# Performance work log

Measured on AMD Instinct MI355X. Metric: run time of the kernel, lower is better.

The kernel has to match this reference:

```python
import jax, jax.numpy as jnp
import numpy as np

B, H, W, C = 16, 64, 64, 768
NB, BS = 8, 96          # n_blocks, block_size (NB*BS == C, no channel padding)
MODES = 8               # (W//2+1)//4


def setup_inputs() -> dict:
    key = jax.random.key(0)
    k = jax.random.split(key, 6)
    x = jax.random.normal(k[0], (B, H * W, C), dtype=jnp.float32)
    block_W = jax.random.normal(k[1], (NB, BS, BS), dtype=jnp.float32) * 0.02
    block_b = jnp.zeros((NB, BS), dtype=jnp.float32)
    gates = jnp.ones((NB,), dtype=jnp.float32) * 0.5
    W_out = jax.random.normal(k[2], (C, NB * BS), dtype=jnp.float32) * 0.02
    b_out = jnp.zeros((C,), dtype=jnp.float32)
    rescale = jnp.asarray(0.1, dtype=jnp.float32)
    return {"x": x, "block_W": block_W, "block_b": block_b, "gates": gates,
            "W_out": W_out, "b_out": b_out, "rescale": rescale}


def reference(x, block_W, block_b, gates, W_out, b_out, rescale):
    Bb, N, Cc = x.shape
    # [B,N,C] -> [B,C,H,W] -> [B,nb,bs,H,W]
    xi = x.reshape(Bb, H, W, Cc).transpose(0, 3, 1, 2).reshape(Bb, NB, BS, H, W)
    xf = jnp.fft.rfft2(xi, norm="ortho")            # [B,nb,bs,H,Wf] complex64
    xt = jnp.transpose(xf[..., :MODES], (0, 1, 3, 4, 2))  # [B,nb,H,m,bs]
    g = jax.nn.sigmoid(gates)[None, :, None, None, None]
    bb = block_b[None, :, None, None, :]
    # block-diagonal real matmul applied to real and imag parts (same W, b)
    out_r = (jnp.einsum("bnhmc,ncd->bnhmd", xt.real, block_W) + bb) * g
    out_i = (jnp.einsum("bnhmc,ncd->bnhmd", xt.imag, block_W) + bb) * g
    out = jax.lax.complex(out_r, out_i)
    out = jnp.transpose(out, (0, 1, 4, 2, 3))       # [B,nb,bs,H,m]
    xf_new = xf.at[..., :MODES].set(out)
    xs = jnp.fft.irfft2(xf_new, s=(H, W), norm="ortho")   # [B,nb,bs,H,W] real
    x_out = xs.reshape(Bb, NB * BS, H, W).transpose(0, 2, 3, 1).reshape(Bb, N, Cc)
    x_proj = (x_out @ W_out.T + b_out) * rescale
    return x_proj + x_out
```

## Files before the change

kernel.cpp:

```cpp
#include <hip/hip_runtime.h>


#define B_ 16
#define H_ 64
#define W_ 64
#define C_ 768
#define NB_ 8
#define BS_ 96
#define MODES_ 8
#define HW_ 4096
#define SPA 776

typedef float f32x4 __attribute__((ext_vector_type(4)));
typedef __bf16 bf16x8 __attribute__((ext_vector_type(8)));

__device__ __forceinline__ float bf2f(unsigned short u){
  unsigned int v = ((unsigned int)u) << 16;
  return __builtin_bit_cast(float, v);
}
__device__ __forceinline__ unsigned short f2bf(float f){
  unsigned int v = __builtin_bit_cast(unsigned int, f);
  v = v + 0x7FFFu + ((v >> 16) & 1u);
  return (unsigned short)(v >> 16);
}

__global__ __launch_bounds__(256) void k_cvt(const float* __restrict__ src,
                                             unsigned short* __restrict__ dst, int n){
  int i = blockIdx.x * 256 + threadIdx.x;
  if (i < n) dst[i] = f2bf(src[i]);
}

__global__ __launch_bounds__(256) void k_prep(const float* __restrict__ bW,
    const float* __restrict__ gates, unsigned short* __restrict__ Wp){
  const int n = blockIdx.x;
  const float g = 1.f / (1.f + expf(-gates[n]));
  for (int i = threadIdx.x; i < BS_ * BS_; i += 256){
    int d = i / BS_, c = i - d * BS_;
    Wp[(size_t)n * BS_ * BS_ + i] = f2bf(g * bW[(size_t)n * BS_ * BS_ + c * BS_ + d]);
  }
}

__global__ __launch_bounds__(256) void k_fwd_w(const float* __restrict__ x, float* __restrict__ S){
  __shared__ float tab[MODES_][W_][2];
  const int tid = threadIdx.x;
  for (int i = tid; i < MODES_ * W_; i += 256){
    int m = i >> 6, w = i & 63;
    float s, c; sincospif((float)((m * w) & 63) * (1.f / 32.f), &s, &c);
    tab[m][w][0] = c; tab[m][w][1] = -s;
  }
  __syncthreads();
  const int b = blockIdx.x >> 6, h = blockIdx.x & 63;
  const float* xr = x + ((size_t)b * HW_ + (size_t)h * W_) * C_;
  float ar[MODES_][3], ai[MODES_][3];
  #pragma unroll
  for (int m = 0; m < MODES_; ++m){
    #pragma unroll
    for (int j = 0; j < 3; ++j){ ar[m][j] = 0.f; ai[m][j] = 0.f; }
  }
  for (int w = 0; w < W_; ++w){
    float xv0 = xr[(size_t)w * C_ + tid];
    float xv1 = xr[(size_t)w * C_ + tid + 256];
    float xv2 = xr[(size_t)w * C_ + tid + 512];
    #pragma unroll
    for (int m = 0; m < MODES_; ++m){
      float c = tab[m][w][0], s = tab[m][w][1];
      ar[m][0] += xv0 * c; ai[m][0] += xv0 * s;
      ar[m][1] += xv1 * c; ai[m][1] += xv1 * s;
      ar[m][2] += xv2 * c; ai[m][2] += xv2 * s;
    }
  }
  float* Sp = S + ((size_t)(b * H_ + h) * (MODES_ * 2)) * C_;
  #pragma unroll
  for (int m = 0; m < MODES_; ++m){
    #pragma unroll
    for (int j = 0; j < 3; ++j){
      Sp[(size_t)(m * 2 + 0) * C_ + tid + j * 256] = ar[m][j];
      Sp[(size_t)(m * 2 + 1) * C_ + tid + j * 256] = ai[m][j];
    }
  }
}

__global__ __launch_bounds__(256) void k_mix2(float* __restrict__ T,
    const unsigned short* __restrict__ Wp, const float* __restrict__ bb,
    const float* __restrict__ gates){
  __shared__ __align__(16) unsigned short sA[16 * SPA];
  const int tid = threadIdx.x;
  float* Tg = T + (size_t)blockIdx.x * 16 * C_;
  #pragma unroll
  for (int r = 0; r < 16; ++r){
    #pragma unroll
    for (int j = 0; j < 3; ++j){
      const int c = tid + 256 * j;
      sA[r * SPA + c] = f2bf(Tg[(size_t)r * C_ + c]);
    }
  }
  __syncthreads();
  const int wv = tid >> 6, ln = tid & 63;
  f32x4 acc[2][6];
  #pragma unroll
  for (int i = 0; i < 2; ++i)
    #pragma unroll
    for (int j = 0; j < 6; ++j) acc[i][j] = {0.f, 0.f, 0.f, 0.f};
  #pragma unroll
  for (int nn = 0; nn < 2; ++nn){
    const int n = wv * 2 + nn, col0 = n * BS_;
    #pragma unroll
    for (int ks = 0; ks < 3; ++ks){
      bf16x8 af = *(const bf16x8*)(sA + (ln & 15) * SPA + col0 + ks * 32 + (ln >> 4) * 8);
      #pragma unroll
      for (int ct = 0; ct < 6; ++ct){
        const unsigned short* bp = Wp + ((size_t)n * BS_ + ct * 16 + (ln & 15)) * BS_
                                      + ks * 32 + (ln >> 4) * 8;
        bf16x8 bf = *(const bf16x8*)bp;
        acc[nn][ct] = __builtin_amdgcn_mfma_f32_16x16x32_bf16(af, bf, acc[nn][ct], 0, 0, 0);
      }
    }
  }
  #pragma unroll
  for (int nn = 0; nn < 2; ++nn){
    const int n = wv * 2 + nn;
    const float g = 1.f / (1.f + expf(-gates[n]));
    #pragma unroll
    for (int ct = 0; ct < 6; ++ct){
      const int dcol = ct * 16 + (ln & 15);
      const int col = n * BS_ + dcol;
      const float gb = g * bb[n * BS_ + dcol];
      #pragma unroll
      for (int j = 0; j < 4; ++j){
        const int row = (ln >> 4) * 4 + j;
        const float wgt = (row < 2 ? 1.f : 2.f) * (1.f / 64.f);
        const size_t o = (size_t)row * C_ + col;
        Tg[o] = (acc[nn][ct][j] + gb - Tg[o]) * wgt;
      }
    }
  }
}

__global__ __launch_bounds__(256) void k_inv_w(const float* __restrict__ Z, const float* __restrict__ x,
                                               unsigned short* __restrict__ xo){
  __shared__ float tab[W_][MODES_][2];
  const int tid = threadIdx.x;
  for (int i = tid; i < W_ * MODES_; i += 256){
    int w = i >> 3, m = i & 7;
    float s, c; sincospif((float)((w * m) & 63) * (1.f / 32.f), &s, &c);
    tab[w][m][0] = c; tab[w][m][1] = s;
  }
  __syncthreads();
  const int b = blockIdx.x >> 6, h = blockIdx.x & 63;
  const float* Zp = Z + ((size_t)(b * H_ + h) * 16) * C_;
  float zr[MODES_][3], zi[MODES_][3];
  #pragma unroll
  for (int m = 0; m < MODES_; ++m){
    #pragma unroll
    for (int j = 0; j < 3; ++j){
      zr[m][j] = Zp[(size_t)(m * 2 + 0) * C_ + tid + j * 256];
      zi[m][j] = Zp[(size_t)(m * 2 + 1) * C_ + tid + j * 256];
    }
  }
  const float* xr = x + ((size_t)b * HW_ + (size_t)h * W_) * C_;
  unsigned short* xop = xo + ((size_t)b * HW_ + (size_t)h * W_) * C_;
  for (int w = 0; w < W_; ++w){
    float y0 = 0.f, y1 = 0.f, y2 = 0.f;
    #pragma unroll
    for (int m = 0; m < MODES_; ++m){
      float cw = tab[w][m][0], sw = tab[w][m][1];
      y0 += zr[m][0] * cw - zi[m][0] * sw;
      y1 += zr[m][1] * cw - zi[m][1] * sw;
      y2 += zr[m][2] * cw - zi[m][2] * sw;
    }
    size_t o = (size_t)w * C_;
    xop[o + tid]       = f2bf(xr[o + tid] + y0);
    xop[o + tid + 256] = f2bf(xr[o + tid + 256] + y1);
    xop[o + tid + 512] = f2bf(xr[o + tid + 512] + y2);
  }
}

__device__ __forceinline__ void async16(const void* g, const void* l){
  __builtin_amdgcn_global_load_lds((__attribute__((address_space(1))) void*)g,
                                   (__attribute__((address_space(3))) void*)l, 16, 0, 0);
}

__global__ __launch_bounds__(256) void k_gemm(const unsigned short* __restrict__ xo,
    const unsigned short* __restrict__ Wb, const float* __restrict__ b_out,
    const float* __restrict__ rescale, float* __restrict__ out){
  __shared__ __align__(16) unsigned short lA[128 * 64];
  __shared__ __align__(16) unsigned short lB[128 * 64];
  const int tid = threadIdx.x;
  const int wv = tid >> 6, ln = tid & 63;
  const int wg = (blockIdx.x & 7) * 384 + (blockIdx.x >> 3);
  const int mt = wg / 6, nt = wg % 6;
  const int mbase = mt * 128, nbase = nt * 128;
  f32x4 acc[4][4];
  #pragma unroll
  for (int i = 0; i < 4; ++i){
    #pragma unroll
    for (int j = 0; j < 4; ++j) acc[i][j] = {0.f, 0.f, 0.f, 0.f};
  }
  const int srow = ln >> 3;
  const int kb_lin = (ln & 7) << 4;
  for (int kt = 0; kt < 12; ++kt){
    __syncthreads();
    const int k0 = kt * 64;
    #pragma unroll
    for (int i = 0; i < 4; ++i){
      const int ch = i * 4 + wv;
      const int row = ch * 8 + srow;
      const int kby = kb_lin ^ ((row & 7) << 4);
      const size_t gA = (size_t)(mbase + row) * C_ + k0 + (kby >> 1);
      const size_t gB = (size_t)(nbase + row) * C_ + k0 + (kby >> 1);
      async16(xo + gA, ((const char*)lA) + ch * 1024);
      async16(Wb + gB, ((const char*)lB) + ch * 1024);
    }
    asm volatile("s_waitcnt vmcnt(0)" ::: "memory");
    __syncthreads();
    const int wr = (wv >> 1) * 64, wc = (wv & 1) * 64;
    #pragma unroll
    for (int kk = 0; kk < 2; ++kk){
      bf16x8 af[4], bg[4];
      #pragma unroll
      for (int mi = 0; mi < 4; ++mi){
        const int row = wr + mi * 16 + (ln & 15);
        int off = (row << 7) + (kk << 6) + ((ln >> 4) << 4);
        off ^= (row & 7) << 4;
        af[mi] = *(const bf16x8*)(((const char*)lA) + off);
      }
      #pragma unroll
      for (int ni = 0; ni < 4; ++ni){
        const int row = wc + ni * 16 + (ln & 15);
        int off = (row << 7) + (kk << 6) + ((ln >> 4) << 4);
        off ^= (row & 7) << 4;
        bg[ni] = *(const bf16x8*)(((const char*)lB) + off);
      }
      #pragma unroll
      for (int mi = 0; mi < 4; ++mi){
        #pragma unroll
        for (int ni = 0; ni < 4; ++ni)
          acc[mi][ni] = __builtin_amdgcn_mfma_f32_16x16x32_bf16(af[mi], bg[ni], acc[mi][ni], 0, 0, 0);
      }
    }
  }
  const float rs = *rescale;
  const int wr = (wv >> 1) * 64, wc = (wv & 1) * 64;
  #pragma unroll
  for (int mi = 0; mi < 4; ++mi){
    const int r0 = mbase + wr + mi * 16 + ((ln >> 4) << 2);
    #pragma unroll
    for (int ni = 0; ni < 4; ++ni){
      const int cidx = nbase + wc + ni * 16 + (ln & 15);
      const float bo = rs * b_out[cidx];
      #pragma unroll
      for (int j = 0; j < 4; ++j){
        const size_t o = (size_t)(r0 + j) * C_ + cidx;
        out[o] = bf2f(xo[o]) + rs * acc[mi][ni][j] + bo;
      }
    }
  }
}

extern "C" void kernel_launch(void* const* d_in, const int* in_sizes, int n_in,
                              void* d_out, int out_size, void* d_ws, size_t ws_size,
                              hipStream_t stream){
  const float* x       = (const float*)d_in[0];
  const float* bW      = (const float*)d_in[1];
  const float* bb      = (const float*)d_in[2];
  const float* gates   = (const float*)d_in[3];
  const float* W_out   = (const float*)d_in[4];
  const float* b_out   = (const float*)d_in[5];
  const float* rescale = (const float*)d_in[6];
  float* out = (float*)d_out;
  char* ws = (char*)d_ws;
  float* S = (float*)(ws);
  unsigned short* xo = (unsigned short*)(ws + 50331648);
  unsigned short* Wb = (unsigned short*)(ws + 50331648 + 100663296);
  unsigned short* Wp = (unsigned short*)(ws + 50331648 + 100663296 + 1179648);

  k_cvt<<<2304, 256, 0, stream>>>(W_out, Wb, C_ * NB_ * BS_);
  k_prep<<<NB_, 256, 0, stream>>>(bW, gates, Wp);
  k_fwd_w<<<B_ * H_, 256, 0, stream>>>(x, S);
  k_mix2<<<B_ * H_, 256, 0, stream>>>(S, Wp, bb, gates);
  k_inv_w<<<B_ * H_, 256, 0, stream>>>(S, x, xo);
  k_gemm<<<(HW_ * B_ / 128) * (C_ / 128), 256, 0, stream>>>(xo, Wb, b_out, rescale, out);
}
```

Before: 358.0 us.

## Double-buffer LDS tiles in output-projection GEMM to overlap loads with MFMA

The GEMM now keeps two LDS buffers for the A and B tiles. It issues the async global-to-LDS load for the next K tile before running the MFMAs on the current one, then waits and synchronises at the end of each iteration. This is meant to hide global load latency behind compute, where the old loop serialised load and compute. In exchange, LDS use doubles to 64KB per block, which can lower occupancy.

```diff
diff --git a/kernel.cpp b/kernel.cpp
--- a/kernel.cpp
+++ b/kernel.cpp
@@ -183,8 +183,8 @@
 __global__ __launch_bounds__(256) void k_gemm(const unsigned short* __restrict__ xo,
     const unsigned short* __restrict__ Wb, const float* __restrict__ b_out,
     const float* __restrict__ rescale, float* __restrict__ out){
-  __shared__ __align__(16) unsigned short lA[128 * 64];
-  __shared__ __align__(16) unsigned short lB[128 * 64];
+  __shared__ __align__(16) unsigned short lA[2][128 * 64];
+  __shared__ __align__(16) unsigned short lB[2][128 * 64];
   const int tid = threadIdx.x;
   const int wv = tid >> 6, ln = tid & 63;
   const int wg = (blockIdx.x & 7) * 384 + (blockIdx.x >> 3);
@@ -192,27 +192,31 @@
   const int mbase = mt * 128, nbase = nt * 128;
   f32x4 acc[4][4];
   #pragma unroll
-  for (int i = 0; i < 4; ++i){
+  for (int i = 0; i < 4; ++i)
     #pragma unroll
     for (int j = 0; j < 4; ++j) acc[i][j] = {0.f, 0.f, 0.f, 0.f};
-  }
   const int srow = ln >> 3;
   const int kb_lin = (ln & 7) << 4;
+
+#define STAGE(pp, kt_) {                                                    \
+    const int k0_ = (kt_) * 64;                                             \
+    _Pragma("unroll")                                                       \
+    for (int i_ = 0; i_ < 4; ++i_){                                         \
+      const int ch_ = i_ * 4 + wv;                                          \
+      const int row_ = ch_ * 8 + srow;                                      \
+      const int kby_ = kb_lin ^ ((row_ & 7) << 4);                          \
+      async16(xo + (size_t)(mbase + row_) * C_ + k0_ + (kby_ >> 1),         \
+              ((const char*)lA[pp]) + ch_ * 1024);                          \
+      async16(Wb + (size_t)(nbase + row_) * C_ + k0_ + (kby_ >> 1),         \
+              ((const char*)lB[pp]) + ch_ * 1024);                          \
+    } }
+
+  STAGE(0, 0);
+  asm volatile("s_waitcnt vmcnt(0)" ::: "memory");
+  __syncthreads();
   for (int kt = 0; kt < 12; ++kt){
-    __syncthreads();
-    const int k0 = kt * 64;
-    #pragma unroll
-    for (int i = 0; i < 4; ++i){
-      const int ch = i * 4 + wv;
-      const int row = ch * 8 + srow;
-      const int kby = kb_lin ^ ((row & 7) << 4);
-      const size_t gA = (size_t)(mbase + row) * C_ + k0 + (kby >> 1);
-      const size_t gB = (size_t)(nbase + row) * C_ + k0 + (kby >> 1);
-      async16(xo + gA, ((const char*)lA) + ch * 1024);
-      async16(Wb + gB, ((const char*)lB) + ch * 1024);
-    }
-    asm volatile("s_waitcnt vmcnt(0)" ::: "memory");
-    __syncthreads();
+    const int p = kt & 1;
+    if (kt + 1 < 12) STAGE(p ^ 1, kt + 1);
     const int wr = (wv >> 1) * 64, wc = (wv & 1) * 64;
     #pragma unroll
     for (int kk = 0; kk < 2; ++kk){
@@ -222,14 +226,14 @@
         const int row = wr + mi * 16 + (ln & 15);
         int off = (row << 7) + (kk << 6) + ((ln >> 4) << 4);
         off ^= (row & 7) << 4;
-        af[mi] = *(const bf16x8*)(((const char*)lA) + off);
+        af[mi] = *(const bf16x8*)(((const char*)lA[p]) + off);
       }
       #pragma unroll
       for (int ni = 0; ni < 4; ++ni){
         const int row = wc + ni * 16 + (ln & 15);
         int off = (row << 7) + (kk << 6) + ((ln >> 4) << 4);
         off ^= (row & 7) << 4;
-        bg[ni] = *(const bf16x8*)(((const char*)lB) + off);
+        bg[ni] = *(const bf16x8*)(((const char*)lB[p]) + off);
       }
       #pragma unroll
       for (int mi = 0; mi < 4; ++mi){
@@ -238,7 +242,10 @@
           acc[mi][ni] = __builtin_amdgcn_mfma_f32_16x16x32_bf16(af[mi], bg[ni], acc[mi][ni], 0, 0, 0);
       }
     }
-  }
+    asm volatile("s_waitcnt vmcnt(0)" ::: "memory");
+    __syncthreads();
+  }
+#undef STAGE
   const float rs = *rescale;
   const int wr = (wv >> 1) * 64, wc = (wv & 1) * 64;
   #pragma unroll
```

Result: slower. 389.8 us (+8.9%).

## Load GEMM MFMA fragments directly from global memory, dropping LDS staging

Applied to the files above, without the earlier changes.

The GEMM kernel no longer stages A and B tiles through shared memory with async global-to-LDS loads and barriers. Each wave now loads its bf16x8 MFMA fragments straight from global memory into registers, one k-tile at a time. This removes the LDS traffic and both __syncthreads per k-step. In exchange, tiles shared between waves are no longer reused through LDS, so each wave re-fetches rows from L2/global. The 16-byte-per-lane loads along rows may also coalesce poorly.

```diff
diff --git a/kernel.cpp b/kernel.cpp
--- a/kernel.cpp
+++ b/kernel.cpp
@@ -175,72 +175,47 @@
   }
 }
 
-__device__ __forceinline__ void async16(const void* g, const void* l){
-  __builtin_amdgcn_global_load_lds((__attribute__((address_space(1))) void*)g,
-                                   (__attribute__((address_space(3))) void*)l, 16, 0, 0);
-}
-
 __global__ __launch_bounds__(256) void k_gemm(const unsigned short* __restrict__ xo,
     const unsigned short* __restrict__ Wb, const float* __restrict__ b_out,
     const float* __restrict__ rescale, float* __restrict__ out){
-  __shared__ __align__(16) unsigned short lA[128 * 64];
-  __shared__ __align__(16) unsigned short lB[128 * 64];
   const int tid = threadIdx.x;
   const int wv = tid >> 6, ln = tid & 63;
   const int wg = (blockIdx.x & 7) * 384 + (blockIdx.x >> 3);
   const int mt = wg / 6, nt = wg % 6;
   const int mbase = mt * 128, nbase = nt * 128;
+  const int wr = (wv >> 1) * 64, wc = (wv & 1) * 64;
   f32x4 acc[4][4];
   #pragma unroll
-  for (int i = 0; i < 4; ++i){
+  for (int i = 0; i < 4; ++i)
     #pragma unroll
     for (int j = 0; j < 4; ++j) acc[i][j] = {0.f, 0.f, 0.f, 0.f};
-  }
-  const int srow = ln >> 3;
-  const int kb_lin = (ln & 7) << 4;
+
+  const unsigned short* Ab = xo + (size_t)(mbase + wr + (ln & 15)) * C_ + ((ln >> 4) * 8);
+  const unsigned short* Bb = Wb + (size_t)(nbase + wc + (ln & 15)) * C_ + ((ln >> 4) * 8);
+
   for (int kt = 0; kt < 12; ++kt){
-    __syncthreads();
-    const int k0 = kt * 64;
-    #pragma unroll
-    for (int i = 0; i < 4; ++i){
-      const int ch = i * 4 + wv;
-      const int row = ch * 8 + srow;
-      const int kby = kb_lin ^ ((row & 7) << 4);
-      const size_t gA = (size_t)(mbase + row) * C_ + k0 + (kby >> 1);
-      const size_t gB = (size_t)(nbase + row) * C_ + k0 + (kby >> 1);
-      async16(xo + gA, ((const char*)lA) + ch * 1024);
-      async16(Wb + gB, ((const char*)lB) + ch * 1024);
-    }
-    asm volatile("s_waitcnt vmcnt(0)" ::: "memory");
-    __syncthreads();
-    const int wr = (wv >> 1) * 64, wc = (wv & 1) * 64;
+    const int koff = kt * 64;
+    bf16x8 af[2][4], bg[2][4];
     #pragma unroll
     for (int kk = 0; kk < 2; ++kk){
-      bf16x8 af[4], bg[4];
       #pragma unroll
       for (int mi = 0; mi < 4; ++mi){
-        const int row = wr + mi * 16 + (ln & 15);
-        int off = (row << 7) + (kk << 6) + ((ln >> 4) << 4);
-        off ^= (row & 7) << 4;
-        af[mi] = *(const bf16x8*)(((const char*)lA) + off);
-      }
-      #pragma unroll
-      for (int ni = 0; ni < 4; ++ni){
-        const int row = wc + ni * 16 + (ln & 15);
-        int off = (row << 7) + (kk << 6) + ((ln >> 4) << 4);
-        off ^= (row & 7) << 4;
-        bg[ni] = *(const bf16x8*)(((const char*)lB) + off);
-      }
+        af[kk][mi] = *(const bf16x8*)(Ab + (size_t)mi * 16 * C_ + koff + kk * 32);
+        bg[kk][mi] = *(const bf16x8*)(Bb + (size_t)mi * 16 * C_ + koff + kk * 32);
+      }
+    }
+    #pragma unroll
+    for (int kk = 0; kk < 2; ++kk){
       #pragma unroll
       for (int mi = 0; mi < 4; ++mi){
         #pragma unroll
         for (int ni = 0; ni < 4; ++ni)
-          acc[mi][ni] = __builtin_amdgcn_mfma_f32_16x16x32_bf16(af[mi], bg[ni], acc[mi][ni], 0, 0, 0);
-      }
-    }
-  }
+          acc[mi][ni] = __builtin_amdgcn_mfma_f32_16x16x32_bf16(af[kk][mi], bg[kk][ni], acc[mi][ni], 0, 0, 0);
+      }
+    }
+  }
+
   const float rs = *rescale;
-  const int wr = (wv >> 1) * 64, wc = (wv & 1) * 64;
   #pragma unroll
   for (int mi = 0; mi < 4; ++mi){
     const int r0 = mbase + wr + mi * 16 + ((ln >> 4) << 2);
```

After: 503.7 us. 1.41x slower.
